# Optimization experiments

Measured on AMD Instinct MI355X. Metric: run time of the kernel, lower is better.

Reference implementation:

```python
import jax, jax.numpy as jnp
import numpy as np

D = 128
N_SRC = 50000
N_DST = 50000
E = 640000
NEG_SLOPE = 0.01  # torch LeakyReLU default


def _lrelu(x):
    return jax.nn.leaky_relu(x, NEG_SLOPE)


def setup_inputs() -> dict:
    key = jax.random.key(0)
    ks = jax.random.split(key, 12)
    s = 1.0 / np.sqrt(D)
    return {
        "feat_src": jax.random.normal(ks[0], (N_SRC, D), jnp.float32),
        "feat_dst": jax.random.normal(ks[1], (N_DST, D), jnp.float32),
        "src_idx": jax.random.randint(ks[2], (E,), 0, N_SRC, jnp.int32),
        "dst_idx": jax.random.randint(ks[3], (E,), 0, N_DST, jnp.int32),
        "W_src": jax.random.uniform(ks[4], (D, D), jnp.float32, -s, s),
        "b_src": jnp.zeros((D,), jnp.float32),
        "W_dst": jax.random.uniform(ks[5], (D, D), jnp.float32, -s, s),
        "b_dst": jnp.zeros((D,), jnp.float32),
        "W_a1": jax.random.uniform(ks[6], (D, D), jnp.float32, -s, s),
        "b_a1": jnp.zeros((D,), jnp.float32),
        "W_a2": jax.random.uniform(ks[7], (D, 1), jnp.float32, -s, s),
        "b_a2": jnp.zeros((1,), jnp.float32),
        "W_out": jax.random.uniform(ks[8], (D, D), jnp.float32, -s, s),
        "b_out": jnp.zeros((D,), jnp.float32),
    }


def reference(feat_src, feat_dst, src_idx, dst_idx,
              W_src, b_src, W_dst, b_dst,
              W_a1, b_a1, W_a2, b_a2, W_out, b_out):
    n_dst = feat_dst.shape[0]
    # node projections (dropout is identity in eval mode)
    hs = feat_src @ W_src + b_src            # [n_src, d]
    hd = feat_dst @ W_dst + b_dst            # [n_dst, d]
    # u_add_v: per-edge feature
    e = hs[src_idx] + hd[dst_idx]            # [E, d]
    # attention MLP: LeakyReLU -> Linear -> LeakyReLU -> Linear(d->1)
    s = _lrelu(_lrelu(e) @ W_a1 + b_a1) @ W_a2 + b_a2  # [E, 1]
    s = s[:, 0]
    # edge softmax grouped by destination node (numerically stable)
    m = jax.ops.segment_max(s, dst_idx, num_segments=n_dst)
    ex = jnp.exp(s - m[dst_idx])
    denom = jax.ops.segment_sum(ex, dst_idx, num_segments=n_dst)
    alpha = ex / denom[dst_idx]              # [E]
    # scale messages and scatter-sum to dst nodes
    n_f = jax.ops.segment_sum(alpha[:, None] * e, dst_idx, num_segments=n_dst)
    return _lrelu(n_f @ W_out + b_out)       # [n_dst, d]
```

## Files before the change

kernel.cpp:

```cpp
#include <hip/hip_runtime.h>
#include <math.h>

#define DD 128
#define NEG 0.01f
#define SCHUNK 4096

typedef __attribute__((ext_vector_type(8))) short short8;
typedef __attribute__((ext_vector_type(4))) float f32x4;

__device__ __forceinline__ float lrelu(float x){ return x > 0.f ? x : NEG * x; }

__device__ __forceinline__ unsigned short f2bf(float f){
    unsigned u = __float_as_uint(f);
    u += 0x7fffu + ((u >> 16) & 1u);
    return (unsigned short)(u >> 16);
}
__device__ __forceinline__ float bf2f(unsigned short h){
    return __uint_as_float(((unsigned)h) << 16);
}

__global__ void init_deg(int* deg, int n_dst){
    int i = blockIdx.x * blockDim.x + threadIdx.x;
    if (i < n_dst) deg[i] = 0;
}

__global__ void hist_kernel(const int* dst, int* deg, int E){
    int i = blockIdx.x * blockDim.x + threadIdx.x;
    if (i < E) atomicAdd(&deg[dst[i]], 1);
}

__global__ __launch_bounds__(1024) void scan1(const int* deg, int* part, int n){
    __shared__ int wsum[16];
    const int tid = threadIdx.x;
    const int lane = tid & 63, wid = tid >> 6;
    int i4 = blockIdx.x * SCHUNK + tid * 4;
    int4 v = make_int4(0, 0, 0, 0);
    if (i4 + 3 < n) v = *(const int4*)(deg + i4);
    else {
        if (i4 + 0 < n) v.x = deg[i4 + 0];
        if (i4 + 1 < n) v.y = deg[i4 + 1];
        if (i4 + 2 < n) v.z = deg[i4 + 2];
        if (i4 + 3 < n) v.w = deg[i4 + 3];
    }
    int t = v.x + v.y + v.z + v.w;
    #pragma unroll
    for (int off = 1; off < 64; off <<= 1) t += __shfl_xor(t, off, 64);
    if (lane == 0) wsum[wid] = t;
    __syncthreads();
    if (tid == 0){
        int s = 0;
        #pragma unroll
        for (int j = 0; j < 16; j++) s += wsum[j];
        part[blockIdx.x] = s;
    }
}

__global__ __launch_bounds__(1024) void scan2(const int* deg, const int* part,
        int* row_off, int* cursor, int n, int nchunks){
    __shared__ int wsum[16];
    const int tid = threadIdx.x;
    const int lane = tid & 63, wid = tid >> 6;
    const int b = blockIdx.x;
    int carry = 0;
    for (int j = 0; j < b; j++) carry += part[j];
    int i4 = b * SCHUNK + tid * 4;
    int4 v = make_int4(0, 0, 0, 0);
    if (i4 + 3 < n) v = *(const int4*)(deg + i4);
    else {
        if (i4 + 0 < n) v.x = deg[i4 + 0];
        if (i4 + 1 < n) v.y = deg[i4 + 1];
        if (i4 + 2 < n) v.z = deg[i4 + 2];
        if (i4 + 3 < n) v.w = deg[i4 + 3];
    }
    int tsum = v.x + v.y + v.z + v.w;
    int x = tsum;
    #pragma unroll
    for (int off = 1; off < 64; off <<= 1){
        int t = __shfl_up(x, off, 64);
        if (lane >= off) x += t;
    }
    if (lane == 63) wsum[wid] = x;
    __syncthreads();
    int wprefix = 0;
    #pragma unroll
    for (int j = 0; j < 16; j++) if (j < wid) wprefix += wsum[j];
    int excl = carry + wprefix + (x - tsum);
    if (i4 + 3 < n){
        int4 o;
        o.x = excl; o.y = excl + v.x; o.z = o.y + v.y; o.w = o.z + v.z;
        *(int4*)(row_off + i4) = o;
        *(int4*)(cursor + i4) = o;
    } else {
        int a = excl;
        if (i4 + 0 < n){ row_off[i4 + 0] = a; cursor[i4 + 0] = a; a += v.x; }
        if (i4 + 1 < n){ row_off[i4 + 1] = a; cursor[i4 + 1] = a; a += v.y; }
        if (i4 + 2 < n){ row_off[i4 + 2] = a; cursor[i4 + 2] = a; a += v.z; }
        if (i4 + 3 < n){ row_off[i4 + 3] = a; cursor[i4 + 3] = a; }
    }
    if (b == 0 && tid == 0){
        int tot = 0;
        for (int j = 0; j < nchunks; j++) tot += part[j];
        row_off[n] = tot;
    }
}

__global__ void scatter_pairs(const int* src, const int* dst, int* cursor,
                              int2* pairs, int* s_srcs, int E){
    int i = blockIdx.x * blockDim.x + threadIdx.x;
    if (i < E){
        int d = dst[i];
        int s = src[i];
        int pos = atomicAdd(&cursor[d], 1);
        pairs[pos] = make_int2(s, d);
        s_srcs[pos] = s;
    }
}

__global__ void pack_weights(const float* Wa1, const float* Wsrc,
                             const float* Wdst, const float* Wout,
                             unsigned short* out){
    int i = blockIdx.x * blockDim.x + threadIdx.x;
    if (i >= 7 * 16384) return;
    int seg = i >> 14, t = i & 16383;
    int j = t & 7, lane = (t >> 3) & 63, nt = (t >> 9) & 7, kc = t >> 12;
    int k = kc * 32 + (lane >> 4) * 8 + j;
    int n = nt * 16 + (lane & 15);
    const float* W = (seg == 0) ? Wa1 : (seg <= 2) ? Wsrc : (seg <= 4) ? Wdst : Wout;
    float w = W[k * DD + n];
    unsigned short hi = f2bf(w);
    unsigned short val = hi;
    if (seg == 2 || seg == 4 || seg == 6) val = f2bf(w - bf2f(hi));
    out[i] = val;
}

__global__ __launch_bounds__(256) void lin2_mfma(
        const float* X1, const unsigned short* W1hi, const unsigned short* W1lo,
        const float* b1, unsigned short* Yb1, int n1, int g1,
        const float* X2, const unsigned short* W2hi, const unsigned short* W2lo,
        const float* b2, float* Y2, unsigned short* Yb2, int n2){
    __shared__ unsigned short sB[2][16384];
    const int tid = threadIdx.x;
    const int second = (blockIdx.x >= g1);
    const float* X = second ? X2 : X1;
    const unsigned short* Whi = second ? W2hi : W1hi;
    const unsigned short* Wlo = second ? W2lo : W1lo;
    const float* b = second ? b2 : b1;
    float* Y = second ? Y2 : (float*)nullptr;
    unsigned short* Yb = second ? Yb2 : Yb1;
    const int nrows = second ? n2 : n1;
    const int bidx = second ? (blockIdx.x - g1) : blockIdx.x;
    {
        const uint4* gh = (const uint4*)Whi;
        const uint4* gl = (const uint4*)Wlo;
        uint4* lh = (uint4*)sB[0];
        uint4* ll = (uint4*)sB[1];
        #pragma unroll
        for (int t = 0; t < 8; t++){
            lh[tid + 256 * t] = gh[tid + 256 * t];
            ll[tid + 256 * t] = gl[tid + 256 * t];
        }
    }
    const int wave = tid >> 6, lane = tid & 63;
    const int qd = lane >> 4, ln16 = lane & 15;
    const int row0 = bidx * 128 + wave * 32;
    int r0 = row0 + ln16;       if (r0 >= nrows) r0 = nrows - 1;
    int r1 = row0 + 16 + ln16;  if (r1 >= nrows) r1 = nrows - 1;
    f32x4 acc[2][8];
    #pragma unroll
    for (int rt = 0; rt < 2; rt++)
        #pragma unroll
        for (int nt = 0; nt < 8; nt++)
            acc[rt][nt] = (f32x4){0.f, 0.f, 0.f, 0.f};
    __syncthreads();
    #pragma unroll
    for (int kc = 0; kc < 4; kc++){
        const int koff = kc * 32 + qd * 8;
        short8 ahi[2], alo[2];
        const float* px[2] = {X + (size_t)r0 * DD + koff, X + (size_t)r1 * DD + koff};
        #pragma unroll
        for (int rt = 0; rt < 2; rt++){
            float4 v0 = *(const float4*)(px[rt]);
            float4 v1 = *(const float4*)(px[rt] + 4);
            float xv[8] = {v0.x, v0.y, v0.z, v0.w, v1.x, v1.y, v1.z, v1.w};
            #pragma unroll
            for (int j = 0; j < 8; j++){
                unsigned short h = f2bf(xv[j]);
                ahi[rt][j] = (short)h;
                alo[rt][j] = (short)f2bf(xv[j] - bf2f(h));
            }
        }
        #pragma unroll
        for (int nt = 0; nt < 8; nt++){
            const int fi = (((kc << 3) + nt) << 6 | lane) << 3;
            short8 bh = *(const short8*)&sB[0][fi];
            short8 bl = *(const short8*)&sB[1][fi];
            #pragma unroll
            for (int rt = 0; rt < 2; rt++){
                acc[rt][nt] = __builtin_amdgcn_mfma_f32_16x16x32_bf16(ahi[rt], bh, acc[rt][nt], 0, 0, 0);
                acc[rt][nt] = __builtin_amdgcn_mfma_f32_16x16x32_bf16(alo[rt], bh, acc[rt][nt], 0, 0, 0);
                acc[rt][nt] = __builtin_amdgcn_mfma_f32_16x16x32_bf16(ahi[rt], bl, acc[rt][nt], 0, 0, 0);
            }
        }
    }
    #pragma unroll
    for (int nt = 0; nt < 8; nt++){
        const int col = nt * 16 + ln16;
        const float bv = b[col];
        #pragma unroll
        for (int rt = 0; rt < 2; rt++){
            #pragma unroll
            for (int r = 0; r < 4; r++){
                int row = row0 + rt * 16 + qd * 4 + r;
                if (row < nrows){
                    float y = acc[rt][nt][r] + bv;
                    if (Y) Y[(size_t)row * DD + col] = y;
                    if (Yb) Yb[(size_t)row * DD + col] = f2bf(y);
                }
            }
        }
    }
}

__global__ __launch_bounds__(256) void lin_mfma(const float* X,
        const unsigned short* Whi, const unsigned short* Wlo, const float* b,
        float* Y, int nrows){
    __shared__ unsigned short sB[2][16384];
    const int tid = threadIdx.x;
    {
        const uint4* gh = (const uint4*)Whi;
        const uint4* gl = (const uint4*)Wlo;
        uint4* lh = (uint4*)sB[0];
        uint4* ll = (uint4*)sB[1];
        #pragma unroll
        for (int t = 0; t < 8; t++){
            lh[tid + 256 * t] = gh[tid + 256 * t];
            ll[tid + 256 * t] = gl[tid + 256 * t];
        }
    }
    const int wave = tid >> 6, lane = tid & 63;
    const int qd = lane >> 4, ln16 = lane & 15;
    const int row0 = blockIdx.x * 128 + wave * 32;
    int r0 = row0 + ln16;       if (r0 >= nrows) r0 = nrows - 1;
    int r1 = row0 + 16 + ln16;  if (r1 >= nrows) r1 = nrows - 1;
    f32x4 acc[2][8];
    #pragma unroll
    for (int rt = 0; rt < 2; rt++)
        #pragma unroll
        for (int nt = 0; nt < 8; nt++)
            acc[rt][nt] = (f32x4){0.f, 0.f, 0.f, 0.f};
    __syncthreads();
    #pragma unroll
    for (int kc = 0; kc < 4; kc++){
        const int koff = kc * 32 + qd * 8;
        short8 ahi[2], alo[2];
        const float* px[2] = {X + (size_t)r0 * DD + koff, X + (size_t)r1 * DD + koff};
        #pragma unroll
        for (int rt = 0; rt < 2; rt++){
            float4 v0 = *(const float4*)(px[rt]);
            float4 v1 = *(const float4*)(px[rt] + 4);
            float xv[8] = {v0.x, v0.y, v0.z, v0.w, v1.x, v1.y, v1.z, v1.w};
            #pragma unroll
            for (int j = 0; j < 8; j++){
                unsigned short h = f2bf(xv[j]);
                ahi[rt][j] = (short)h;
                alo[rt][j] = (short)f2bf(xv[j] - bf2f(h));
            }
        }
        #pragma unroll
        for (int nt = 0; nt < 8; nt++){
            const int fi = (((kc << 3) + nt) << 6 | lane) << 3;
            short8 bh = *(const short8*)&sB[0][fi];
            short8 bl = *(const short8*)&sB[1][fi];
            #pragma unroll
            for (int rt = 0; rt < 2; rt++){
                acc[rt][nt] = __builtin_amdgcn_mfma_f32_16x16x32_bf16(ahi[rt], bh, acc[rt][nt], 0, 0, 0);
                acc[rt][nt] = __builtin_amdgcn_mfma_f32_16x16x32_bf16(alo[rt], bh, acc[rt][nt], 0, 0, 0);
                acc[rt][nt] = __builtin_amdgcn_mfma_f32_16x16x32_bf16(ahi[rt], bl, acc[rt][nt], 0, 0, 0);
            }
        }
    }
    #pragma unroll
    for (int nt = 0; nt < 8; nt++){
        const int col = nt * 16 + ln16;
        const float bv = b[col];
        #pragma unroll
        for (int rt = 0; rt < 2; rt++){
            #pragma unroll
            for (int r = 0; r < 4; r++){
                int row = row0 + rt * 16 + qd * 4 + r;
                if (row < nrows){
                    float y = acc[rt][nt][r] + bv;
                    Y[(size_t)row * DD + col] = lrelu(y);
                }
            }
        }
    }
}

__device__ __forceinline__ short8 make_afrag(const unsigned short* ph, const unsigned short* pd){
    uint4 a = *(const uint4*)ph;
    uint4 b = *(const uint4*)pd;
    unsigned au[4] = {a.x, a.y, a.z, a.w};
    unsigned bu[4] = {b.x, b.y, b.z, b.w};
    int4 out;
    int* op = (int*)&out;
    #pragma unroll
    for (int i = 0; i < 4; i++){
        float h0 = __uint_as_float(au[i] << 16);
        float h1 = __uint_as_float(au[i] & 0xffff0000u);
        float g0 = __uint_as_float(bu[i] << 16);
        float g1 = __uint_as_float(bu[i] & 0xffff0000u);
        float e0 = lrelu(h0 + g0);
        float e1 = lrelu(h1 + g1);
        op[i] = (int)((__float_as_uint(e0) >> 16) | (__float_as_uint(e1) & 0xffff0000u));
    }
    return *(short8*)&out;
}

__global__ __launch_bounds__(256) void edge_score_mfma(
        const unsigned short* hs_b, const unsigned short* hd_b,
        const int2* pairs,
        const unsigned short* wa1p, const float* ba1,
        const float* Wa2, const float* ba2,
        float* s_w, int E){
    __shared__ unsigned short sB[16384];
    const int tid = threadIdx.x;
    {
        const uint4* g = (const uint4*)wa1p;
        uint4* l = (uint4*)sB;
        #pragma unroll
        for (int t = 0; t < 8; t++) l[tid + 256 * t] = g[tid + 256 * t];
    }
    const int wave = tid >> 6, lane = tid & 63;
    const int qd = lane >> 4, ln16 = lane & 15;
    const int e0 = blockIdx.x * 128 + wave * 32;
    float b1v[8], w2v[8];
    #pragma unroll
    for (int nt = 0; nt < 8; nt++){
        b1v[nt] = ba1[nt * 16 + ln16];
        w2v[nt] = Wa2[nt * 16 + ln16];
    }
    const float b2 = ba2[0];
    __syncthreads();
    for (int rt = 0; rt < 2; rt++){
        int eid = e0 + rt * 16 + ln16;
        if (eid >= E) eid = E - 1;
        const int2 pp = pairs[eid];
        f32x4 acc[8];
        #pragma unroll
        for (int nt = 0; nt < 8; nt++) acc[nt] = (f32x4){0.f, 0.f, 0.f, 0.f};
        #pragma unroll
        for (int kc = 0; kc < 4; kc++){
            const int koff = kc * 32 + qd * 8;
            short8 af = make_afrag(hs_b + (size_t)pp.x * DD + koff,
                                   hd_b + (size_t)pp.y * DD + koff);
            #pragma unroll
            for (int nt = 0; nt < 8; nt++){
                short8 bf = *(const short8*)&sB[(((kc << 3) + nt) << 6 | lane) << 3];
                acc[nt] = __builtin_amdgcn_mfma_f32_16x16x32_bf16(af, bf, acc[nt], 0, 0, 0);
            }
        }
        float p[4] = {0.f, 0.f, 0.f, 0.f};
        #pragma unroll
        for (int nt = 0; nt < 8; nt++)
            #pragma unroll
            for (int r = 0; r < 4; r++){
                float z = acc[nt][r] + b1v[nt];
                z = z > 0.f ? z : NEG * z;
                p[r] += z * w2v[nt];
            }
        #pragma unroll
        for (int r = 0; r < 4; r++){
            float v = p[r];
            #pragma unroll
            for (int off = 1; off < 16; off <<= 1) v += __shfl_xor(v, off, 64);
            p[r] = expf(v + b2);
        }
        if (ln16 == 0){
            int row = e0 + rt * 16 + qd * 4;
            #pragma unroll
            for (int r = 0; r < 4; r++)
                if (row + r < E) s_w[row + r] = p[r];
        }
    }
}

__global__ __launch_bounds__(256) void agg_softmax(const unsigned short* hs_b,
        const unsigned short* hd_b, const int* row_off, const int* s_srcs,
        const float* s_w, float* nf, int n_dst){
    const int w = (blockIdx.x * blockDim.x + threadIdx.x) >> 6;
    const int lane = threadIdx.x & 63;
    if (w >= n_dst) return;
    const int beg = row_off[w], end = row_off[w + 1];
    float2 acc = make_float2(0.f, 0.f);
    float sa = 0.f;
    int e = beg;
    for (; e + 3 < end; e += 4){
        float w0 = s_w[e], w1 = s_w[e + 1], w2 = s_w[e + 2], w3 = s_w[e + 3];
        int s0 = s_srcs[e], s1 = s_srcs[e + 1], s2 = s_srcs[e + 2], s3 = s_srcs[e + 3];
        ushort2 u0 = *(const ushort2*)(hs_b + (size_t)s0 * DD + lane * 2);
        ushort2 u1 = *(const ushort2*)(hs_b + (size_t)s1 * DD + lane * 2);
        ushort2 u2 = *(const ushort2*)(hs_b + (size_t)s2 * DD + lane * 2);
        ushort2 u3 = *(const ushort2*)(hs_b + (size_t)s3 * DD + lane * 2);
        acc.x += w0 * bf2f(u0.x) + w1 * bf2f(u1.x) + w2 * bf2f(u2.x) + w3 * bf2f(u3.x);
        acc.y += w0 * bf2f(u0.y) + w1 * bf2f(u1.y) + w2 * bf2f(u2.y) + w3 * bf2f(u3.y);
        sa += (w0 + w1) + (w2 + w3);
    }
    for (; e < end; e++){
        float w0 = s_w[e];
        int s0 = s_srcs[e];
        ushort2 u0 = *(const ushort2*)(hs_b + (size_t)s0 * DD + lane * 2);
        acc.x += w0 * bf2f(u0.x);
        acc.y += w0 * bf2f(u0.y);
        sa += w0;
    }
    const float inv = (end > beg) ? 1.f / sa : 0.f;
    ushort2 hu = *(const ushort2*)(hd_b + (size_t)w * DD + lane * 2);
    const float hx = (end > beg) ? bf2f(hu.x) : 0.f;
    const float hy = (end > beg) ? bf2f(hu.y) : 0.f;
    float2 out;
    out.x = acc.x * inv + hx;
    out.y = acc.y * inv + hy;
    *(float2*)(nf + (size_t)w * DD + lane * 2) = out;
}

extern "C" void kernel_launch(void* const* d_in, const int* in_sizes, int n_in,
                              void* d_out, int out_size, void* d_ws, size_t ws_size,
                              hipStream_t stream){
    const float* feat_src = (const float*)d_in[0];
    const float* feat_dst = (const float*)d_in[1];
    const int*   src_idx  = (const int*)d_in[2];
    const int*   dst_idx  = (const int*)d_in[3];
    const float* W_src = (const float*)d_in[4];
    const float* b_src = (const float*)d_in[5];
    const float* W_dst = (const float*)d_in[6];
    const float* b_dst = (const float*)d_in[7];
    const float* W_a1  = (const float*)d_in[8];
    const float* b_a1  = (const float*)d_in[9];
    const float* W_a2  = (const float*)d_in[10];
    const float* b_a2  = (const float*)d_in[11];
    const float* W_out = (const float*)d_in[12];
    const float* b_out = (const float*)d_in[13];
    const int n_src = in_sizes[0] / DD;
    const int n_dst = in_sizes[1] / DD;
    const int E = in_sizes[2];
    const int nchunks = (n_dst + SCHUNK - 1) / SCHUNK;

    char* p = (char*)d_ws;
    unsigned short* hs_b = (unsigned short*)p;  p += (size_t)n_src * DD * 2;
    unsigned short* hd_b = (unsigned short*)p;  p += (size_t)n_dst * DD * 2;
    unsigned short* wpack = (unsigned short*)p; p += 7 * 16384 * 2;
    float* s_w = (float*)p;                     p += (size_t)E * 4;
    int2* pairs = (int2*)p;                     p += (size_t)E * 8;
    int* s_srcs = (int*)p;                      p += (size_t)E * 4;
    int* deg = (int*)p;                         p += (size_t)n_dst * 4;
    int* cursor = (int*)p;                      p += (size_t)n_dst * 4;
    int* part = (int*)p;                        p += 64 * 4;
    int* row_off = (int*)p;                     p += ((size_t)n_dst + 1) * 4;
    float* nf = (float*)d_out;

    const unsigned short* wa1p    = wpack;
    const unsigned short* wsrc_hi = wpack + 1 * 16384;
    const unsigned short* wsrc_lo = wpack + 2 * 16384;
    const unsigned short* wdst_hi = wpack + 3 * 16384;
    const unsigned short* wdst_lo = wpack + 4 * 16384;
    const unsigned short* wout_hi = wpack + 5 * 16384;
    const unsigned short* wout_lo = wpack + 6 * 16384;

    init_deg<<<(n_dst + 255) / 256, 256, 0, stream>>>(deg, n_dst);
    hist_kernel<<<(E + 255) / 256, 256, 0, stream>>>(dst_idx, deg, E);
    scan1<<<nchunks, 1024, 0, stream>>>(deg, part, n_dst);
    scan2<<<nchunks, 1024, 0, stream>>>(deg, part, row_off, cursor, n_dst, nchunks);
    pack_weights<<<(7 * 16384 + 255) / 256, 256, 0, stream>>>(W_a1, W_src, W_dst, W_out, wpack);
    scatter_pairs<<<(E + 255) / 256, 256, 0, stream>>>(src_idx, dst_idx, cursor,
                                                       pairs, s_srcs, E);
    const int g1 = (n_src + 127) / 128;
    const int g2 = (n_dst + 127) / 128;
    lin2_mfma<<<g1 + g2, 256, 0, stream>>>(feat_src, wsrc_hi, wsrc_lo, b_src, hs_b, n_src, g1,
                                           feat_dst, wdst_hi, wdst_lo, b_dst,
                                           (float*)nullptr, hd_b, n_dst);
    edge_score_mfma<<<(E + 127) / 128, 256, 0, stream>>>(hs_b, hd_b, pairs, wa1p, b_a1,
                                                         W_a2, b_a2, s_w, E);
    agg_softmax<<<((size_t)n_dst * 64 + 255) / 256, 256, 0, stream>>>(hs_b, hd_b, row_off,
                                                                      s_srcs, s_w, nf, n_dst);
    lin_mfma<<<g2, 256, 0, stream>>>(nf, wout_hi, wout_lo, b_out, nf, n_dst);
}
```

Before: 330.3 us.

## Switch intermediates and MFMA to fp16, fuse hist with weight pack, double edge tile

```diff
diff --git a/kernel.cpp b/kernel.cpp
--- a/kernel.cpp
+++ b/kernel.cpp
@@ -5,28 +5,40 @@
 #define NEG 0.01f
 #define SCHUNK 4096
 
-typedef __attribute__((ext_vector_type(8))) short short8;
+typedef __attribute__((ext_vector_type(8))) _Float16 half8;
 typedef __attribute__((ext_vector_type(4))) float f32x4;
 
 __device__ __forceinline__ float lrelu(float x){ return x > 0.f ? x : NEG * x; }
 
-__device__ __forceinline__ unsigned short f2bf(float f){
-    unsigned u = __float_as_uint(f);
-    u += 0x7fffu + ((u >> 16) & 1u);
-    return (unsigned short)(u >> 16);
-}
-__device__ __forceinline__ float bf2f(unsigned short h){
-    return __uint_as_float(((unsigned)h) << 16);
-}
-
-__global__ void init_deg(int* deg, int n_dst){
-    int i = blockIdx.x * blockDim.x + threadIdx.x;
-    if (i < n_dst) deg[i] = 0;
-}
-
-__global__ void hist_kernel(const int* dst, int* deg, int E){
-    int i = blockIdx.x * blockDim.x + threadIdx.x;
-    if (i < E) atomicAdd(&deg[dst[i]], 1);
+__device__ __forceinline__ unsigned short h2u(_Float16 h){
+    union { _Float16 h; unsigned short u; } v; v.h = h; return v.u;
+}
+__device__ __forceinline__ _Float16 u2h(unsigned short u){
+    union { unsigned short u; _Float16 h; } v; v.u = u; return v.h;
+}
+
+__global__ void hist_pack(const int* dst, int* deg, int E, int nhist,
+                          const float* Wa1, const float* Wsrc,
+                          const float* Wdst, const float* Wout,
+                          unsigned short* wpack){
+    const int bid = blockIdx.x;
+    if (bid < nhist){
+        int i = bid * 256 + threadIdx.x;
+        if (i < E) atomicAdd(&deg[dst[i]], 1);
+    } else {
+        int i = (bid - nhist) * 256 + threadIdx.x;
+        if (i >= 7 * 16384) return;
+        int seg = i >> 14, t = i & 16383;
+        int j = t & 7, lane = (t >> 3) & 63, nt = (t >> 9) & 7, kc = t >> 12;
+        int k = kc * 32 + (lane >> 4) * 8 + j;
+        int n = nt * 16 + (lane & 15);
+        const float* W = (seg == 0) ? Wa1 : (seg <= 2) ? Wsrc : (seg <= 4) ? Wdst : Wout;
+        float w = W[k * DD + n];
+        _Float16 hi = (_Float16)w;
+        unsigned short val = h2u(hi);
+        if (seg == 2 || seg == 4 || seg == 6) val = h2u((_Float16)(w - (float)hi));
+        wpack[i] = val;
+    }
 }
 
 __global__ __launch_bounds__(1024) void scan1(const int* deg, int* part, int n){
@@ -116,28 +128,11 @@
     }
 }
 
-__global__ void pack_weights(const float* Wa1, const float* Wsrc,
-                             const float* Wdst, const float* Wout,
-                             unsigned short* out){
-    int i = blockIdx.x * blockDim.x + threadIdx.x;
-    if (i >= 7 * 16384) return;
-    int seg = i >> 14, t = i & 16383;
-    int j = t & 7, lane = (t >> 3) & 63, nt = (t >> 9) & 7, kc = t >> 12;
-    int k = kc * 32 + (lane >> 4) * 8 + j;
-    int n = nt * 16 + (lane & 15);
-    const float* W = (seg == 0) ? Wa1 : (seg <= 2) ? Wsrc : (seg <= 4) ? Wdst : Wout;
-    float w = W[k * DD + n];
-    unsigned short hi = f2bf(w);
-    unsigned short val = hi;
-    if (seg == 2 || seg == 4 || seg == 6) val = f2bf(w - bf2f(hi));
-    out[i] = val;
-}
-
 __global__ __launch_bounds__(256) void lin2_mfma(
         const float* X1, const unsigned short* W1hi, const unsigned short* W1lo,
         const float* b1, unsigned short* Yb1, int n1, int g1,
         const float* X2, const unsigned short* W2hi, const unsigned short* W2lo,
-        const float* b2, float* Y2, unsigned short* Yb2, int n2){
+        const float* b2, unsigned short* Yb2, int n2){
     __shared__ unsigned short sB[2][16384];
     const int tid = threadIdx.x;
     const int second = (blockIdx.x >= g1);
@@ -145,7 +140,6 @@
     const unsigned short* Whi = second ? W2hi : W1hi;
     const unsigned short* Wlo = second ? W2lo : W1lo;
     const float* b = second ? b2 : b1;
-    float* Y = second ? Y2 : (float*)nullptr;
     unsigned short* Yb = second ? Yb2 : Yb1;
     const int nrows = second ? n2 : n1;
     const int bidx = second ? (blockIdx.x - g1) : blockIdx.x;
@@ -175,7 +169,7 @@
     #pragma unroll
     for (int kc = 0; kc < 4; kc++){
         const int koff = kc * 32 + qd * 8;
-        short8 ahi[2], alo[2];
+        half8 ahi[2], alo[2];
         const float* px[2] = {X + (size_t)r0 * DD + koff, X + (size_t)r1 * DD + koff};
         #pragma unroll
         for (int rt = 0; rt < 2; rt++){
@@ -184,21 +178,21 @@
             float xv[8] = {v0.x, v0.y, v0.z, v0.w, v1.x, v1.y, v1.z, v1.w};
             #pragma unroll
             for (int j = 0; j < 8; j++){
-                unsigned short h = f2bf(xv[j]);
-                ahi[rt][j] = (short)h;
-                alo[rt][j] = (short)f2bf(xv[j] - bf2f(h));
+                _Float16 h = (_Float16)xv[j];
+                ahi[rt][j] = h;
+                alo[rt][j] = (_Float16)(xv[j] - (float)h);
             }
         }
         #pragma unroll
         for (int nt = 0; nt < 8; nt++){
             const int fi = (((kc << 3) + nt) << 6 | lane) << 3;
-            short8 bh = *(const short8*)&sB[0][fi];
-            short8 bl = *(const short8*)&sB[1][fi];
+            half8 bh = *(const half8*)&sB[0][fi];
+            half8 bl = *(const half8*)&sB[1][fi];
             #pragma unroll
             for (int rt = 0; rt < 2; rt++){
-                acc[rt][nt] = __builtin_amdgcn_mfma_f32_16x16x32_bf16(ahi[rt], bh, acc[rt][nt], 0, 0, 0);
-                acc[rt][nt] = __builtin_amdgcn_mfma_f32_16x16x32_bf16(alo[rt], bh, acc[rt][nt], 0, 0, 0);
-                acc[rt][nt] = __builtin_amdgcn_mfma_f32_16x16x32_bf16(ahi[rt], bl, acc[rt][nt], 0, 0, 0);
+                acc[rt][nt] = __builtin_amdgcn_mfma_f32_16x16x32_f16(ahi[rt], bh, acc[rt][nt], 0, 0, 0);
+                acc[rt][nt] = __builtin_amdgcn_mfma_f32_16x16x32_f16(alo[rt], bh, acc[rt][nt], 0, 0, 0);
+                acc[rt][nt] = __builtin_amdgcn_mfma_f32_16x16x32_f16(ahi[rt], bl, acc[rt][nt], 0, 0, 0);
             }
         }
     }
@@ -213,8 +207,7 @@
                 int row = row0 + rt * 16 + qd * 4 + r;
                 if (row < nrows){
                     float y = acc[rt][nt][r] + bv;
-                    if (Y) Y[(size_t)row * DD + col] = y;
-                    if (Yb) Yb[(size_t)row * DD + col] = f2bf(y);
+                    Yb[(size_t)row * DD + col] = h2u((_Float16)y);
                 }
             }
         }
@@ -252,7 +245,7 @@
     #pragma unroll
     for (int kc = 0; kc < 4; kc++){
         const int koff = kc * 32 + qd * 8;
-        short8 ahi[2], alo[2];
+        half8 ahi[2], alo[2];
         const float* px[2] = {X + (size_t)r0 * DD + koff, X + (size_t)r1 * DD + koff};
         #pragma unroll
         for (int rt = 0; rt < 2; rt++){
@@ -261,21 +254,21 @@
             float xv[8] = {v0.x, v0.y, v0.z, v0.w, v1.x, v1.y, v1.z, v1.w};
             #pragma unroll
             for (int j = 0; j < 8; j++){
-                unsigned short h = f2bf(xv[j]);
-                ahi[rt][j] = (short)h;
-                alo[rt][j] = (short)f2bf(xv[j] - bf2f(h));
+                _Float16 h = (_Float16)xv[j];
+                ahi[rt][j] = h;
+                alo[rt][j] = (_Float16)(xv[j] - (float)h);
             }
         }
         #pragma unroll
         for (int nt = 0; nt < 8; nt++){
             const int fi = (((kc << 3) + nt) << 6 | lane) << 3;
-            short8 bh = *(const short8*)&sB[0][fi];
-            short8 bl = *(const short8*)&sB[1][fi];
+            half8 bh = *(const half8*)&sB[0][fi];
+            half8 bl = *(const half8*)&sB[1][fi];
             #pragma unroll
             for (int rt = 0; rt < 2; rt++){
-                acc[rt][nt] = __builtin_amdgcn_mfma_f32_16x16x32_bf16(ahi[rt], bh, acc[rt][nt], 0, 0, 0);
-                acc[rt][nt] = __builtin_amdgcn_mfma_f32_16x16x32_bf16(alo[rt], bh, acc[rt][nt], 0, 0, 0);
-                acc[rt][nt] = __builtin_amdgcn_mfma_f32_16x16x32_bf16(ahi[rt], bl, acc[rt][nt], 0, 0, 0);
+                acc[rt][nt] = __builtin_amdgcn_mfma_f32_16x16x32_f16(ahi[rt], bh, acc[rt][nt], 0, 0, 0);
+                acc[rt][nt] = __builtin_amdgcn_mfma_f32_16x16x32_f16(alo[rt], bh, acc[rt][nt], 0, 0, 0);
+                acc[rt][nt] = __builtin_amdgcn_mfma_f32_16x16x32_f16(ahi[rt], bl, acc[rt][nt], 0, 0, 0);
             }
         }
     }
@@ -297,28 +290,19 @@
     }
 }
 
-__device__ __forceinline__ short8 make_afrag(const unsigned short* ph, const unsigned short* pd){
-    uint4 a = *(const uint4*)ph;
-    uint4 b = *(const uint4*)pd;
-    unsigned au[4] = {a.x, a.y, a.z, a.w};
-    unsigned bu[4] = {b.x, b.y, b.z, b.w};
-    int4 out;
-    int* op = (int*)&out;
-    #pragma unroll
-    for (int i = 0; i < 4; i++){
-        float h0 = __uint_as_float(au[i] << 16);
-        float h1 = __uint_as_float(au[i] & 0xffff0000u);
-        float g0 = __uint_as_float(bu[i] << 16);
-        float g1 = __uint_as_float(bu[i] & 0xffff0000u);
-        float e0 = lrelu(h0 + g0);
-        float e1 = lrelu(h1 + g1);
-        op[i] = (int)((__float_as_uint(e0) >> 16) | (__float_as_uint(e1) & 0xffff0000u));
-    }
-    return *(short8*)&out;
+__device__ __forceinline__ half8 make_afrag(const unsigned short* ph, const unsigned short* pd){
+    half8 a = *(const half8*)ph;
+    half8 b = *(const half8*)pd;
+    half8 s = a + b;
+    half8 l = s * (_Float16)0.01f;
+    half8 r;
+    #pragma unroll
+    for (int i = 0; i < 8; i++) r[i] = (s[i] > (_Float16)0.f) ? s[i] : l[i];
+    return r;
 }
 
 __global__ __launch_bounds__(256) void edge_score_mfma(
-        const unsigned short* hs_b, const unsigned short* hd_b,
+        const unsigned short* hs_h, const unsigned short* hd_h,
         const int2* pairs,
         const unsigned short* wa1p, const float* ba1,
         const float* Wa2, const float* ba2,
@@ -333,7 +317,6 @@
     }
     const int wave = tid >> 6, lane = tid & 63;
     const int qd = lane >> 4, ln16 = lane & 15;
-    const int e0 = blockIdx.x * 128 + wave * 32;
     float b1v[8], w2v[8];
     #pragma unroll
     for (int nt = 0; nt < 8; nt++){
@@ -342,51 +325,54 @@
     }
     const float b2 = ba2[0];
     __syncthreads();
-    for (int rt = 0; rt < 2; rt++){
-        int eid = e0 + rt * 16 + ln16;
-        if (eid >= E) eid = E - 1;
-        const int2 pp = pairs[eid];
-        f32x4 acc[8];
-        #pragma unroll
-        for (int nt = 0; nt < 8; nt++) acc[nt] = (f32x4){0.f, 0.f, 0.f, 0.f};
-        #pragma unroll
-        for (int kc = 0; kc < 4; kc++){
-            const int koff = kc * 32 + qd * 8;
-            short8 af = make_afrag(hs_b + (size_t)pp.x * DD + koff,
-                                   hd_b + (size_t)pp.y * DD + koff);
-            #pragma unroll
-            for (int nt = 0; nt < 8; nt++){
-                short8 bf = *(const short8*)&sB[(((kc << 3) + nt) << 6 | lane) << 3];
-                acc[nt] = __builtin_amdgcn_mfma_f32_16x16x32_bf16(af, bf, acc[nt], 0, 0, 0);
-            }
-        }
-        float p[4] = {0.f, 0.f, 0.f, 0.f};
-        #pragma unroll
-        for (int nt = 0; nt < 8; nt++)
+    for (int half = 0; half < 2; half++){
+        const int e0 = blockIdx.x * 256 + half * 128 + wave * 32;
+        for (int rt = 0; rt < 2; rt++){
+            int eid = e0 + rt * 16 + ln16;
+            if (eid >= E) eid = E - 1;
+            const int2 pp = pairs[eid];
+            f32x4 acc[8];
+            #pragma unroll
+            for (int nt = 0; nt < 8; nt++) acc[nt] = (f32x4){0.f, 0.f, 0.f, 0.f};
+            #pragma unroll
+            for (int kc = 0; kc < 4; kc++){
+                const int koff = kc * 32 + qd * 8;
+                half8 af = make_afrag(hs_h + (size_t)pp.x * DD + koff,
+                                      hd_h + (size_t)pp.y * DD + koff);
+                #pragma unroll
+                for (int nt = 0; nt < 8; nt++){
+                    half8 bf = *(const half8*)&sB[(((kc << 3) + nt) << 6 | lane) << 3];
+                    acc[nt] = __builtin_amdgcn_mfma_f32_16x16x32_f16(af, bf, acc[nt], 0, 0, 0);
+                }
+            }
+            float p[4] = {0.f, 0.f, 0.f, 0.f};
+            #pragma unroll
+            for (int nt = 0; nt < 8; nt++)
+                #pragma unroll
+                for (int r = 0; r < 4; r++){
+                    float z = acc[nt][r] + b1v[nt];
+                    z = z > 0.f ? z : NEG * z;
+                    p[r] += z * w2v[nt];
+                }
             #pragma unroll
             for (int r = 0; r < 4; r++){
-                float z = acc[nt][r] + b1v[nt];
-                z = z > 0.f ? z : NEG * z;
-                p[r] += z * w2v[nt];
-            }
-        #pragma unroll
-        for (int r = 0; r < 4; r++){
-            float v = p[r];
-            #pragma unroll
-            for (int off = 1; off < 16; off <<= 1) v += __shfl_xor(v, off, 64);
-            p[r] = expf(v + b2);
-        }
-        if (ln16 == 0){
-            int row = e0 + rt * 16 + qd * 4;
-            #pragma unroll
-            for (int r = 0; r < 4; r++)
-                if (row + r < E) s_w[row + r] = p[r];
-        }
-    }
-}
-
-__global__ __launch_bounds__(256) void agg_softmax(const unsigned short* hs_b,
-        const unsigned short* hd_b, const int* row_off, const int* s_srcs,
+                float v = p[r];
+                #pragma unroll
+                for (int off = 1; off < 16; off <<= 1) v += __shfl_xor(v, off, 64);
+                p[r] = expf(v + b2);
+            }
+            if (ln16 == 0){
+                int row = e0 + rt * 16 + qd * 4;
+                #pragma unroll
+                for (int r = 0; r < 4; r++)
+                    if (row + r < E) s_w[row + r] = p[r];
+            }
+        }
+    }
+}
+
+__global__ __launch_bounds__(256) void agg_softmax(const unsigned short* hs_h,
+        const unsigned short* hd_h, const int* row_off, const int* s_srcs,
         const float* s_w, float* nf, int n_dst){
     const int w = (blockIdx.x * blockDim.x + threadIdx.x) >> 6;
     const int lane = threadIdx.x & 63;
@@ -398,26 +384,28 @@
     for (; e + 3 < end; e += 4){
         float w0 = s_w[e], w1 = s_w[e + 1], w2 = s_w[e + 2], w3 = s_w[e + 3];
         int s0 = s_srcs[e], s1 = s_srcs[e + 1], s2 = s_srcs[e + 2], s3 = s_srcs[e + 3];
-        ushort2 u0 = *(const ushort2*)(hs_b + (size_t)s0 * DD + lane * 2);
-        ushort2 u1 = *(const ushort2*)(hs_b + (size_t)s1 * DD + lane * 2);
-        ushort2 u2 = *(const ushort2*)(hs_b + (size_t)s2 * DD + lane * 2);
-        ushort2 u3 = *(const ushort2*)(hs_b + (size_t)s3 * DD + lane * 2);
-        acc.x += w0 * bf2f(u0.x) + w1 * bf2f(u1.x) + w2 * bf2f(u2.x) + w3 * bf2f(u3.x);
-        acc.y += w0 * bf2f(u0.y) + w1 * bf2f(u1.y) + w2 * bf2f(u2.y) + w3 * bf2f(u3.y);
+        ushort2 u0 = *(const ushort2*)(hs_h + (size_t)s0 * DD + lane * 2);
+        ushort2 u1 = *(const ushort2*)(hs_h + (size_t)s1 * DD + lane * 2);
+        ushort2 u2 = *(const ushort2*)(hs_h + (size_t)s2 * DD + lane * 2);
+        ushort2 u3 = *(const ushort2*)(hs_h + (size_t)s3 * DD + lane * 2);
+        acc.x += w0 * (float)u2h(u0.x) + w1 * (float)u2h(u1.x)
+               + w2 * (float)u2h(u2.x) + w3 * (float)u2h(u3.x);
+        acc.y += w0 * (float)u2h(u0.y) + w1 * (float)u2h(u1.y)
+               + w2 * (float)u2h(u2.y) + w3 * (float)u2h(u3.y);
         sa += (w0 + w1) + (w2 + w3);
     }
     for (; e < end; e++){
         float w0 = s_w[e];
         int s0 = s_srcs[e];
-        ushort2 u0 = *(const ushort2*)(hs_b + (size_t)s0 * DD + lane * 2);
-        acc.x += w0 * bf2f(u0.x);
-        acc.y += w0 * bf2f(u0.y);
+        ushort2 u0 = *(const ushort2*)(hs_h + (size_t)s0 * DD + lane * 2);
+        acc.x += w0 * (float)u2h(u0.x);
+        acc.y += w0 * (float)u2h(u0.y);
         sa += w0;
     }
     const float inv = (end > beg) ? 1.f / sa : 0.f;
-    ushort2 hu = *(const ushort2*)(hd_b + (size_t)w * DD + lane * 2);
-    const float hx = (end > beg) ? bf2f(hu.x) : 0.f;
-    const float hy = (end > beg) ? bf2f(hu.y) : 0.f;
+    ushort2 hu = *(const ushort2*)(hd_h + (size_t)w * DD + lane * 2);
+    const float hx = (end > beg) ? (float)u2h(hu.x) : 0.f;
+    const float hy = (end > beg) ? (float)u2h(hu.y) : 0.f;
     float2 out;
     out.x = acc.x * inv + hx;
     out.y = acc.y * inv + hy;
@@ -447,8 +435,8 @@
     const int nchunks = (n_dst + SCHUNK - 1) / SCHUNK;
 
     char* p = (char*)d_ws;
-    unsigned short* hs_b = (unsigned short*)p;  p += (size_t)n_src * DD * 2;
-    unsigned short* hd_b = (unsigned short*)p;  p += (size_t)n_dst * DD * 2;
+    unsigned short* hs_h = (unsigned short*)p;  p += (size_t)n_src * DD * 2;
+    unsigned short* hd_h = (unsigned short*)p;  p += (size_t)n_dst * DD * 2;
     unsigned short* wpack = (unsigned short*)p; p += 7 * 16384 * 2;
     float* s_w = (float*)p;                     p += (size_t)E * 4;
     int2* pairs = (int2*)p;                     p += (size_t)E * 8;
@@ -467,21 +455,22 @@
     const unsigned short* wout_hi = wpack + 5 * 16384;
     const unsigned short* wout_lo = wpack + 6 * 16384;
 
-    init_deg<<<(n_dst + 255) / 256, 256, 0, stream>>>(deg, n_dst);
-    hist_kernel<<<(E + 255) / 256, 256, 0, stream>>>(dst_idx, deg, E);
+    hipMemsetAsync(deg, 0, (size_t)n_dst * 4, stream);
+    const int nhist = (E + 255) / 256;
+    const int npack = (7 * 16384 + 255) / 256;
+    hist_pack<<<nhist + npack, 256, 0, stream>>>(dst_idx, deg, E, nhist,
+                                                 W_a1, W_src, W_dst, W_out, wpack);
     scan1<<<nchunks, 1024, 0, stream>>>(deg, part, n_dst);
     scan2<<<nchunks, 1024, 0, stream>>>(deg, part, row_off, cursor, n_dst, nchunks);
-    pack_weights<<<(7 * 16384 + 255) / 256, 256, 0, stream>>>(W_a1, W_src, W_dst, W_out, wpack);
     scatter_pairs<<<(E + 255) / 256, 256, 0, stream>>>(src_idx, dst_idx, cursor,
                                                        pairs, s_srcs, E);
     const int g1 = (n_src + 127) / 128;
     const int g2 = (n_dst + 127) / 128;
-    lin2_mfma<<<g1 + g2, 256, 0, stream>>>(feat_src, wsrc_hi, wsrc_lo, b_src, hs_b, n_src, g1,
-                                           feat_dst, wdst_hi, wdst_lo, b_dst,
-                                           (float*)nullptr, hd_b, n_dst);
-    edge_score_mfma<<<(E + 127) / 128, 256, 0, stream>>>(hs_b, hd_b, pairs, wa1p, b_a1,
+    lin2_mfma<<<g1 + g2, 256, 0, stream>>>(feat_src, wsrc_hi, wsrc_lo, b_src, hs_h, n_src, g1,
+                                           feat_dst, wdst_hi, wdst_lo, b_dst, hd_h, n_dst);
+    edge_score_mfma<<<(E + 255) / 256, 256, 0, stream>>>(hs_h, hd_h, pairs, wa1p, b_a1,
                                                          W_a2, b_a2, s_w, E);
-    agg_softmax<<<((size_t)n_dst * 64 + 255) / 256, 256, 0, stream>>>(hs_b, hd_b, row_off,
+    agg_softmax<<<((size_t)n_dst * 64 + 255) / 256, 256, 0, stream>>>(hs_h, hd_h, row_off,
                                                                       s_srcs, s_w, nf, n_dst);
     lin_mfma<<<g2, 256, 0, stream>>>(nf, wout_hi, wout_lo, b_out, nf, n_dst);
 }
```

Result: no change. 325.0 us (-1.6%).
